# Performance work log

Hardware: AMD Instinct MI355X
Metric: run time of the kernel (lower is better)

Reference implementation:

```python
import jax, jax.numpy as jnp
import numpy as np

EPS = 1e-5
NUM_HEADS = 20


def ln(x, w, b=None):
    m = x.mean(-1, keepdims=True)
    v = x.var(-1, keepdims=True)
    y = (x - m) * jax.lax.rsqrt(v + EPS) * w
    return y + b if b is not None else y


def rotate_half(t):
    t1, t2 = jnp.split(t, 2, axis=-1)
    return jnp.concatenate([-t2, t1], axis=-1)


def setup_inputs() -> dict:
    key = jax.random.key(0)
    B, S, E = 8, 1024, 1280  # 8 packed sequences of length 1024, ESM-2 650M width
    T = B * S
    ks = jax.random.split(key, 6)
    scale = (1.0 / E) ** 0.5  # ~xavier scale
    w = lambda k: jax.random.normal(k, (E, E), jnp.float32) * scale
    return {
        "x": jax.random.normal(ks[0], (T, E), jnp.float32),
        "cu_lens": jnp.arange(B + 1, dtype=jnp.int32) * S,
        "max_len": S,
        "norm_w": jnp.ones((E,), jnp.float32),
        "norm_b": jnp.zeros((E,), jnp.float32),
        "Wq": w(ks[1]),
        "Wk": w(ks[2]),
        "Wv": w(ks[3]),
        "Wout": w(ks[4]),
        "lnq_w": jnp.ones((E,), jnp.float32),
        "lnk_w": jnp.ones((E,), jnp.float32),
    }


def reference(x, cu_lens, max_len, norm_w, norm_b, Wq, Wk, Wv, Wout, lnq_w, lnk_w):
    T, E = x.shape
    H = NUM_HEADS
    D = E // H

    # pre-norm + separate Q/K/V projections (bias=False)
    h = ln(x, norm_w, norm_b)
    q = ln(h @ Wq.T, lnq_w)   # per-head-stack LayerNorm on q (no bias)
    k = ln(h @ Wk.T, lnk_w)
    v = h @ Wv.T

    q = q.reshape(T, H, D)
    k = k.reshape(T, H, D)
    v = v.reshape(T, H, D)

    # rotary embedding: positions restart at each sequence boundary (cu_lens)
    tok = jnp.arange(T)
    seg = jnp.searchsorted(cu_lens, tok, side="right") - 1
    pos = (tok - cu_lens[seg]).astype(jnp.float32)
    inv_freq = 1.0 / (10000.0 ** (jnp.arange(0, D, 2, dtype=jnp.float32) / D))
    f = pos[:, None] * inv_freq[None, :]                      # [T, D/2]
    cos = jnp.concatenate([jnp.cos(f), jnp.cos(f)], -1)[:, None, :]  # [T,1,D]
    sin = jnp.concatenate([jnp.sin(f), jnp.sin(f)], -1)[:, None, :]
    q = q * cos + rotate_half(q) * sin
    k = k * cos + rotate_half(k) * sin

    # varlen flash attention; sequences are equal-length here so reshape to
    # [B,S,...] which exactly honors the block-diagonal (no cross-sequence) mask
    B = cu_lens.shape[0] - 1
    S = T // B
    qb = q.reshape(B, S, H, D)
    kb = k.reshape(B, S, H, D)
    vb = v.reshape(B, S, H, D)

    scores = jnp.einsum("bqhd,bkhd->bhqk", qb, kb) * (D ** -0.5)
    attn = jax.nn.softmax(scores, axis=-1)
    o = jnp.einsum("bhqk,bkhd->bqhd", attn, vb).reshape(T, E)
    return o @ Wout.T
```

## Files before the change

kernel.cpp:

```cpp
#include <hip/hip_runtime.h>
#include <hip/hip_bf16.h>
#include <math.h>

#define NH 20
#define HD 64
#define E_DIM 1280
#define T_TOK 8192
#define NSEQ 8
#define N4 (E_DIM * E_DIM / 4)

#define SCALE_LOG2 0.1803368801111204f
#define THR_RAW 44.3614f

typedef unsigned short u16;
typedef unsigned int u32;
typedef __attribute__((ext_vector_type(8))) short bf16x8;
typedef __attribute__((ext_vector_type(4))) float f32x4;
typedef __attribute__((ext_vector_type(16))) float f32x16;

__device__ __forceinline__ float bf2f(u16 h) {
  union { float f; unsigned u; } c; c.u = ((unsigned)h) << 16; return c.f;
}
__device__ __forceinline__ u16 f2bf(float f) {
  union { float f; unsigned u; } c; c.f = f;
  unsigned u = c.u;
  return (u16)((u + 0x7fffu + ((u >> 16) & 1u)) >> 16);
}
__device__ __forceinline__ u32 cvtpk(float lo, float hi) {
  u32 r;
  asm("v_cvt_pk_bf16_f32 %0, %1, %2" : "=v"(r) : "v"(lo), "v"(hi));
  return r;
}

__device__ __forceinline__ void gld_lds16(const void* g, void* l) {
  __builtin_amdgcn_global_load_lds((const __attribute__((address_space(1))) void*)g,
                                   (__attribute__((address_space(3))) void*)l,
                                   16, 0, 0);
}

__global__ __launch_bounds__(256) void cvt_all(const float* __restrict__ Wq,
                                               const float* __restrict__ Wk,
                                               const float* __restrict__ Wv,
                                               const float* __restrict__ Wo,
                                               u16* __restrict__ wqkv,
                                               u16* __restrict__ wo) {
  int i = blockIdx.x * 256 + threadIdx.x;
  if (i >= 4 * N4) return;
  int r = i / N4;
  int l = i - r * N4;
  const float* src = (r == 0) ? Wq : (r == 1) ? Wk : (r == 2) ? Wv : Wo;
  float4 v = ((const float4*)src)[l];
  ushort4 ov;
  ov.x = f2bf(v.x); ov.y = f2bf(v.y); ov.z = f2bf(v.z); ov.w = f2bf(v.w);
  if (r < 3) ((ushort4*)wqkv)[(size_t)r * N4 + l] = ov;
  else       ((ushort4*)wo)[l] = ov;
}

__global__ __launch_bounds__(256) void rope_tab_kernel(float2* __restrict__ tab) {
  int i = blockIdx.x * 256 + threadIdx.x;
  if (i >= 1024 * 32) return;
  int pos = i >> 5, dm = i & 31;
  float freq = exp2f(-(float)dm * (13.287712379549449f / 32.0f));
  float f = (float)pos * freq;
  tab[i] = make_float2(cosf(f), sinf(f));
}

__global__ __launch_bounds__(320) void ln_x_kernel(const float* __restrict__ x,
                                                   const float* __restrict__ w,
                                                   const float* __restrict__ b,
                                                   u16* __restrict__ h) {
  const int row = blockIdx.x;
  const int tid = threadIdx.x;
  const float4 xv = ((const float4*)(x + (size_t)row * E_DIM))[tid];
  float s  = xv.x + xv.y + xv.z + xv.w;
  float s2 = xv.x*xv.x + xv.y*xv.y + xv.z*xv.z + xv.w*xv.w;
#pragma unroll
  for (int m = 1; m < 64; m <<= 1) { s += __shfl_xor(s, m); s2 += __shfl_xor(s2, m); }
  __shared__ float ss[5], ss2[5];
  if ((tid & 63) == 0) { ss[tid >> 6] = s; ss2[tid >> 6] = s2; }
  __syncthreads();
  s  = ss[0] + ss[1] + ss[2] + ss[3] + ss[4];
  s2 = ss2[0] + ss2[1] + ss2[2] + ss2[3] + ss2[4];
  const float mean = s * (1.0f / E_DIM);
  const float var  = s2 * (1.0f / E_DIM) - mean * mean;
  const float rstd = rsqrtf(var + 1e-5f);
  const float4 wv = ((const float4*)w)[tid];
  const float4 bv = ((const float4*)b)[tid];
  ushort4 o;
  o.x = f2bf((xv.x - mean) * rstd * wv.x + bv.x);
  o.y = f2bf((xv.y - mean) * rstd * wv.y + bv.y);
  o.z = f2bf((xv.z - mean) * rstd * wv.z + bv.z);
  o.w = f2bf((xv.w - mean) * rstd * wv.w + bv.w);
  ((ushort4*)(h + (size_t)row * E_DIM))[tid] = o;
}

__global__ __launch_bounds__(320) void ln_rope_kernel(const u16* __restrict__ pre,
                                                      const float* __restrict__ w,
                                                      const int* __restrict__ cu,
                                                      const float2* __restrict__ tab,
                                                      u16* __restrict__ outq) {
  const int row = blockIdx.x;
  const int tid = threadIdx.x;
  __shared__ float y[E_DIM];
  const ushort4 qv = ((const ushort4*)(pre + (size_t)row * E_DIM))[tid];
  float v0 = bf2f(qv.x), v1 = bf2f(qv.y), v2 = bf2f(qv.z), v3 = bf2f(qv.w);
  float s  = v0 + v1 + v2 + v3;
  float s2 = v0*v0 + v1*v1 + v2*v2 + v3*v3;
#pragma unroll
  for (int m = 1; m < 64; m <<= 1) { s += __shfl_xor(s, m); s2 += __shfl_xor(s2, m); }
  __shared__ float ss[5], ss2[5];
  if ((tid & 63) == 0) { ss[tid >> 6] = s; ss2[tid >> 6] = s2; }
  __syncthreads();
  s  = ss[0] + ss[1] + ss[2] + ss[3] + ss[4];
  s2 = ss2[0] + ss2[1] + ss2[2] + ss2[3] + ss2[4];
  const float mean = s * (1.0f / E_DIM);
  const float var  = s2 * (1.0f / E_DIM) - mean * mean;
  const float rstd = rsqrtf(var + 1e-5f);
  const int e0 = tid * 4;
  const float4 wv = ((const float4*)w)[tid];
  y[e0 + 0] = (v0 - mean) * rstd * wv.x;
  y[e0 + 1] = (v1 - mean) * rstd * wv.y;
  y[e0 + 2] = (v2 - mean) * rstd * wv.z;
  y[e0 + 3] = (v3 - mean) * rstd * wv.w;
  __syncthreads();
  int seg = 0;
#pragma unroll
  for (int bb = 1; bb < NSEQ + 1; bb++) if (cu[bb] <= row) seg = bb;
  const int pos = row - cu[seg];
  const int d0 = e0 & 63;
  const int hbase = e0 - d0;
  const float4* tp = (const float4*)(tab + pos * 32 + (d0 & 31));
  const float4 t0 = tp[0], t1 = tp[1];
  const float cs_[4] = {t0.x, t0.z, t1.x, t1.z};
  const float sn_[4] = {t0.y, t0.w, t1.y, t1.w};
  const bool lo = (d0 < 32);
  ushort4 o;
#pragma unroll
  for (int i = 0; i < 4; i++) {
    const int d = d0 + i;
    float r;
    if (lo) r = y[hbase + d] * cs_[i] - y[hbase + d + 32] * sn_[i];
    else    r = y[hbase + d] * cs_[i] + y[hbase + d - 32] * sn_[i];
    ((u16*)&o)[i] = f2bf(r);
  }
  ((ushort4*)(outq + (size_t)row * E_DIM))[tid] = o;
}

__global__ __launch_bounds__(256) void gemm_qkv(const u16* __restrict__ A,
                                                const u16* __restrict__ B,
                                                u16* __restrict__ preq,
                                                u16* __restrict__ prek,
                                                u16* __restrict__ vT) {
  __shared__ u16 As[128 * 64];
  __shared__ u16 Bs[128 * 64];
  const int K = E_DIM;
  const int tid = threadIdx.x;
  const int wid = tid >> 6;
  const int lane = tid & 63;
  const int l16 = lane & 15, lq = lane >> 4;
  const int bm = blockIdx.x & 63;
  const int bn = blockIdx.x >> 6;
  const int m0 = bm << 7, n0 = bn << 7;
  const int wr = (wid >> 1) << 6;
  const int wc = (wid & 1) << 6;

  f32x4 acc[4][4] = {};
  const int rbase = tid >> 3;
  const int csw = (((tid & 7) ^ ((tid >> 3) & 7)) << 3);
  const int sw = l16 & 7;
  const int ldst = (wid << 6) * 8;

  for (int k0 = 0; k0 < K; k0 += 64) {
#pragma unroll
    for (int j = 0; j < 4; j++) {
      const int row = j * 32 + rbase;
      gld_lds16(A + (size_t)(m0 + row) * K + k0 + csw, &As[(size_t)(j * 2048) + ldst]);
      gld_lds16(B + (size_t)(n0 + row) * K + k0 + csw, &Bs[(size_t)(j * 2048) + ldst]);
    }
    __syncthreads();
#pragma unroll
    for (int kk = 0; kk < 2; kk++) {
      bf16x8 af[4], bfr[4];
#pragma unroll
      for (int mi = 0; mi < 4; mi++)
        af[mi] = *(const bf16x8*)(&As[(wr + mi * 16 + l16) * 64 + ((((kk << 2) | lq) ^ sw) << 3)]);
#pragma unroll
      for (int ni = 0; ni < 4; ni++)
        bfr[ni] = *(const bf16x8*)(&Bs[(wc + ni * 16 + l16) * 64 + ((((kk << 2) | lq) ^ sw) << 3)]);
#pragma unroll
      for (int mi = 0; mi < 4; mi++)
#pragma unroll
        for (int ni = 0; ni < 4; ni++)
          acc[mi][ni] = __builtin_amdgcn_mfma_f32_16x16x32_bf16(af[mi], bfr[ni], acc[mi][ni], 0, 0, 0);
    }
    __syncthreads();
  }

  if (n0 < 2560) {
    u16* dst; int c0;
    if (n0 < 1280) { dst = preq; c0 = n0; }
    else           { dst = prek; c0 = n0 - 1280; }
#pragma unroll
    for (int mi = 0; mi < 4; mi++)
#pragma unroll
      for (int j = 0; j < 4; j++) {
        const size_t rowo = (size_t)(m0 + wr + mi * 16 + lq * 4 + j) * E_DIM;
#pragma unroll
        for (int ni = 0; ni < 4; ni++)
          dst[rowo + c0 + wc + ni * 16 + l16] = f2bf(acc[mi][ni][j]);
      }
  } else {
    const int c0 = n0 - 2560;
#pragma unroll
    for (int mi = 0; mi < 4; mi++)
#pragma unroll
      for (int ni = 0; ni < 4; ni++) {
        ushort4 pkt;
        pkt.x = f2bf(acc[mi][ni][0]); pkt.y = f2bf(acc[mi][ni][1]);
        pkt.z = f2bf(acc[mi][ni][2]); pkt.w = f2bf(acc[mi][ni][3]);
        const size_t off = (size_t)(c0 + wc + ni * 16 + l16) * T_TOK + (m0 + wr + mi * 16 + lq * 4);
        *(ushort4*)(vT + off) = pkt;
      }
  }
}

__global__ __launch_bounds__(256) void gemm_out(const u16* __restrict__ A,
                                                const u16* __restrict__ B,
                                                float* __restrict__ C) {
  __shared__ u16 As[128 * 64];
  __shared__ u16 Bs[128 * 64];
  const int K = E_DIM, N = E_DIM;
  const int tid = threadIdx.x;
  const int wid = tid >> 6;
  const int lane = tid & 63;
  const int l16 = lane & 15, lq = lane >> 4;
  const int bm = blockIdx.x & 63;
  const int bn = blockIdx.x >> 6;
  const int m0 = bm << 7, n0 = bn << 7;
  const int wr = (wid >> 1) << 6;
  const int wc = (wid & 1) << 6;

  f32x4 acc[4][4] = {};
  const int rbase = tid >> 3;
  const int csw = (((tid & 7) ^ ((tid >> 3) & 7)) << 3);
  const int sw = l16 & 7;
  const int ldst = (wid << 6) * 8;

  for (int k0 = 0; k0 < K; k0 += 64) {
#pragma unroll
    for (int j = 0; j < 4; j++) {
      const int row = j * 32 + rbase;
      gld_lds16(A + (size_t)(m0 + row) * K + k0 + csw, &As[(size_t)(j * 2048) + ldst]);
      gld_lds16(B + (size_t)(n0 + row) * K + k0 + csw, &Bs[(size_t)(j * 2048) + ldst]);
    }
    __syncthreads();
#pragma unroll
    for (int kk = 0; kk < 2; kk++) {
      bf16x8 af[4], bfr[4];
#pragma unroll
      for (int mi = 0; mi < 4; mi++)
        af[mi] = *(const bf16x8*)(&As[(wr + mi * 16 + l16) * 64 + ((((kk << 2) | lq) ^ sw) << 3)]);
#pragma unroll
      for (int ni = 0; ni < 4; ni++)
        bfr[ni] = *(const bf16x8*)(&Bs[(wc + ni * 16 + l16) * 64 + ((((kk << 2) | lq) ^ sw) << 3)]);
#pragma unroll
      for (int mi = 0; mi < 4; mi++)
#pragma unroll
        for (int ni = 0; ni < 4; ni++)
          acc[mi][ni] = __builtin_amdgcn_mfma_f32_16x16x32_bf16(af[mi], bfr[ni], acc[mi][ni], 0, 0, 0);
    }
    __syncthreads();
  }

#pragma unroll
  for (int mi = 0; mi < 4; mi++)
#pragma unroll
    for (int j = 0; j < 4; j++) {
      const size_t rowo = (size_t)(m0 + wr + mi * 16 + lq * 4 + j) * N;
#pragma unroll
      for (int ni = 0; ni < 4; ni++)
        C[rowo + n0 + wc + ni * 16 + l16] = acc[mi][ni][j];
    }
}

__global__ __launch_bounds__(256) void attn_kernel(const u16* __restrict__ q,
                                                   const u16* __restrict__ k,
                                                   const u16* __restrict__ vT,
                                                   const int* __restrict__ cu,
                                                   u16* __restrict__ o) {
  const int bx = blockIdx.x;
  const int qt = bx & 7;
  const int hh = (bx >> 3) % NH;
  const int b  = bx / (8 * NH);
  const int base = cu[b];
  const int nkt  = (cu[b + 1] - base) >> 6;
  const int tid  = threadIdx.x;
  const int wid  = tid >> 6, lane = tid & 63;
  const int l31  = lane & 31, hi = lane >> 5;

  __shared__ u16 Ks[2][64 * 64];
  __shared__ u16 Vs[2][64 * 64];

  const int qrow = base + qt * 128 + wid * 32 + l31;
  bf16x8 qf[4];
#pragma unroll
  for (int kk = 0; kk < 4; kk++)
    qf[kk] = *(const bf16x8*)(q + (size_t)qrow * E_DIM + hh * 64 + kk * 16 + hi * 8);

  f32x16 acc0 = {}, acc1 = {};
  float mrow = -1e30f, lrow = 0.f;

  const int r0 = tid >> 3;
  const int chs = tid & 7;
  const int cs0 = (chs ^ (r0 & 7)) << 3;
  const int r1 = r0 + 32;
  const int cs1 = (chs ^ (r1 & 7)) << 3;
  const u16* kg0 = k  + (size_t)(base + r0) * E_DIM + hh * 64 + cs0;
  const u16* kg1 = k  + (size_t)(base + r1) * E_DIM + hh * 64 + cs1;
  const u16* vg0 = vT + (size_t)(hh * 64 + r0) * T_TOK + base + cs0;
  const u16* vg1 = vT + (size_t)(hh * 64 + r1) * T_TOK + base + cs1;
  const int ldsoff = wid * 512;

  gld_lds16(kg0, &Ks[0][ldsoff]);
  gld_lds16(kg1, &Ks[0][2048 + ldsoff]);
  gld_lds16(vg0, &Vs[0][ldsoff]);
  gld_lds16(vg1, &Vs[0][2048 + ldsoff]);
  __syncthreads();

  int cur = 0;
  for (int kt = 0; kt < nkt; kt++) {
    if (kt + 1 < nkt) {
      const size_t ko = (size_t)(kt + 1) * 64 * E_DIM;
      const int vo = (kt + 1) * 64;
      u16* kd = Ks[cur ^ 1];
      u16* vd = Vs[cur ^ 1];
      gld_lds16(kg0 + ko, kd + ldsoff);
      gld_lds16(kg1 + ko, kd + 2048 + ldsoff);
      gld_lds16(vg0 + vo, vd + ldsoff);
      gld_lds16(vg1 + vo, vd + 2048 + ldsoff);
    }
    const u16* Kc = Ks[cur];
    const u16* Vc = Vs[cur];

    f32x16 S0 = {}, S1 = {};
#pragma unroll
    for (int kk = 0; kk < 4; kk++) {
      const int c0 = (((kk << 1) | hi) ^ (l31 & 7)) << 3;
      const bf16x8 kf0 = *(const bf16x8*)(Kc + l31 * 64 + c0);
      const bf16x8 kf1 = *(const bf16x8*)(Kc + (32 + l31) * 64 + c0);
      S0 = __builtin_amdgcn_mfma_f32_32x32x16_bf16(kf0, qf[kk], S0, 0, 0, 0);
      S1 = __builtin_amdgcn_mfma_f32_32x32x16_bf16(kf1, qf[kk], S1, 0, 0, 0);
    }

    float tm = S0[0];
#pragma unroll
    for (int r = 1; r < 16; r++) tm = fmaxf(tm, S0[r]);
#pragma unroll
    for (int r = 0; r < 16; r++) tm = fmaxf(tm, S1[r]);
    tm = fmaxf(tm, __shfl_xor(tm, 32));

    if (__any(tm > mrow + THR_RAW)) {
      const float nm = fmaxf(mrow, tm);
      const float al = exp2f((mrow - nm) * SCALE_LOG2);
      mrow = nm;
      lrow *= al;
#pragma unroll
      for (int r = 0; r < 16; r++) {
        const float as = __shfl(al, (r & 3) + 8 * (r >> 2) + 4 * hi);
        acc0[r] *= as;
        acc1[r] *= as;
      }
    }
    const float ms = mrow * SCALE_LOG2;
    float rs = 0.f;
#pragma unroll
    for (int r = 0; r < 16; r++) {
      S0[r] = exp2f(fmaf(S0[r], SCALE_LOG2, -ms));
      rs += S0[r];
    }
#pragma unroll
    for (int r = 0; r < 16; r++) {
      S1[r] = exp2f(fmaf(S1[r], SCALE_LOG2, -ms));
      rs += S1[r];
    }
    rs += __shfl_xor(rs, 32);
    lrow += rs;

    u32 pw[4][4];
#pragma unroll
    for (int ks = 0; ks < 4; ks++) {
      const int g = (ks & 1) << 3;
      u32 A0, A1, B0, B1;
      if (ks < 2) {
        A0 = cvtpk(S0[g + 0], S0[g + 1]); A1 = cvtpk(S0[g + 2], S0[g + 3]);
        B0 = cvtpk(S0[g + 4], S0[g + 5]); B1 = cvtpk(S0[g + 6], S0[g + 7]);
      } else {
        A0 = cvtpk(S1[g + 0], S1[g + 1]); A1 = cvtpk(S1[g + 2], S1[g + 3]);
        B0 = cvtpk(S1[g + 4], S1[g + 5]); B1 = cvtpk(S1[g + 6], S1[g + 7]);
      }
      asm("v_permlane32_swap_b32 %0, %1" : "+v"(A0), "+v"(B0));
      asm("v_permlane32_swap_b32 %0, %1" : "+v"(A1), "+v"(B1));
      pw[ks][0] = A0; pw[ks][1] = A1; pw[ks][2] = B0; pw[ks][3] = B1;
    }

#pragma unroll
    for (int ks = 0; ks < 4; ks++) {
      const bf16x8 pa = *(const bf16x8*)&pw[ks][0];
      const int c0 = (((ks << 1) | hi) ^ (l31 & 7)) << 3;
      const bf16x8 vf0 = *(const bf16x8*)(Vc + l31 * 64 + c0);
      const bf16x8 vf1 = *(const bf16x8*)(Vc + (32 + l31) * 64 + c0);
      acc0 = __builtin_amdgcn_mfma_f32_32x32x16_bf16(pa, vf0, acc0, 0, 0, 0);
      acc1 = __builtin_amdgcn_mfma_f32_32x32x16_bf16(pa, vf1, acc1, 0, 0, 0);
    }
    __syncthreads();
    cur ^= 1;
  }

  const float linv = 1.0f / lrow;
  const int tok0 = base + qt * 128 + wid * 32;
#pragma unroll
  for (int r = 0; r < 16; r++) {
    const int qr = (r & 3) + 8 * (r >> 2) + 4 * hi;
    const float ls = __shfl(linv, qr);
    const size_t ro = (size_t)(tok0 + qr) * E_DIM + hh * 64 + l31;
    o[ro]      = f2bf(acc0[r] * ls);
    o[ro + 32] = f2bf(acc1[r] * ls);
  }
}

extern "C" void kernel_launch(void* const* d_in, const int* in_sizes, int n_in,
                              void* d_out, int out_size, void* d_ws, size_t ws_size,
                              hipStream_t stream) {
  const float* x      = (const float*)d_in[0];
  const int*   cu     = (const int*)d_in[1];
  const float* norm_w = (const float*)d_in[3];
  const float* norm_b = (const float*)d_in[4];
  const float* Wq     = (const float*)d_in[5];
  const float* Wk     = (const float*)d_in[6];
  const float* Wv     = (const float*)d_in[7];
  const float* Wo     = (const float*)d_in[8];
  const float* lnq    = (const float*)d_in[9];
  const float* lnk    = (const float*)d_in[10];
  float* out = (float*)d_out;

  const size_t EE2 = (size_t)E_DIM * E_DIM * 2;
  const size_t TE2 = (size_t)T_TOK * E_DIM * 2;
  char* p = (char*)d_ws;
  u16* wqkv = (u16*)p; p += 3 * EE2;
  u16* wo_b = (u16*)p; p += EE2;
  u16* h_b  = (u16*)p; p += TE2;
  u16* preq = (u16*)p; p += TE2;
  u16* prek = (u16*)p; p += TE2;
  u16* vT_b = (u16*)p; p += TE2;
  float2* tab = (float2*)p; p += 1024 * 32 * sizeof(float2);

  cvt_all<<<(4 * N4 + 255) / 256, 256, 0, stream>>>(Wq, Wk, Wv, Wo, wqkv, wo_b);
  rope_tab_kernel<<<128, 256, 0, stream>>>(tab);
  ln_x_kernel<<<T_TOK, 320, 0, stream>>>(x, norm_w, norm_b, h_b);

  gemm_qkv<<<64 * 30, 256, 0, stream>>>(h_b, wqkv, preq, prek, vT_b);

  ln_rope_kernel<<<T_TOK, 320, 0, stream>>>(preq, lnq, cu, tab, preq);
  ln_rope_kernel<<<T_TOK, 320, 0, stream>>>(prek, lnk, cu, tab, prek);

  attn_kernel<<<8 * NH * NSEQ, 256, 0, stream>>>(preq, prek, vT_b, cu, h_b);

  gemm_out<<<64 * 10, 256, 0, stream>>>(h_b, wo_b, out);
}
```

Baseline: 297.2 us.

## Replace both GEMMs with 256x256 double-buffered 8-wave pipelined template

Merges the QKV and output projection GEMMs into one templated kernel with 256x256 tiles, 512 threads and double-buffered LDS. Global-to-LDS loads are interleaved with MFMA quarter-blocks under explicit vmcnt/lgkmcnt waits, barriers and setprio. The goal is to hide load latency and raise data reuse per block. In exchange it uses 128KB of LDS per block with fewer blocks, and the out GEMM launches only 160 blocks on a chip with 256 CUs, which leaves many CUs idle.

```diff
diff --git a/kernel.cpp b/kernel.cpp
--- a/kernel.cpp
+++ b/kernel.cpp
@@ -37,6 +37,12 @@
                                    (__attribute__((address_space(3))) void*)l,
                                    16, 0, 0);
 }
+
+#define BARR() __builtin_amdgcn_s_barrier()
+#define LGKM0() do { asm volatile("s_waitcnt lgkmcnt(0)" ::: "memory"); \
+                     __builtin_amdgcn_sched_barrier(0); } while (0)
+#define VMC4() asm volatile("s_waitcnt vmcnt(4)" ::: "memory")
+#define VMC0() asm volatile("s_waitcnt vmcnt(0)" ::: "memory")
 
 __global__ __launch_bounds__(256) void cvt_all(const float* __restrict__ Wq,
                                                const float* __restrict__ Wk,
@@ -146,141 +152,150 @@
   ((ushort4*)(outq + (size_t)row * E_DIM))[tid] = o;
 }
 
-__global__ __launch_bounds__(256) void gemm_qkv(const u16* __restrict__ A,
-                                                const u16* __restrict__ B,
-                                                u16* __restrict__ preq,
-                                                u16* __restrict__ prek,
-                                                u16* __restrict__ vT) {
-  __shared__ u16 As[128 * 64];
-  __shared__ u16 Bs[128 * 64];
-  const int K = E_DIM;
+template <int MODE, int K>
+__global__ __launch_bounds__(512) void gemm256(const u16* __restrict__ A,
+                                               const u16* __restrict__ B,
+                                               u16* __restrict__ preq,
+                                               u16* __restrict__ prek,
+                                               u16* __restrict__ vT,
+                                               float* __restrict__ Cf) {
+  __shared__ u16 As[2][16384];
+  __shared__ u16 Bs[2][16384];
   const int tid = threadIdx.x;
-  const int wid = tid >> 6;
-  const int lane = tid & 63;
+  const int wid = tid >> 6, lane = tid & 63;
   const int l16 = lane & 15, lq = lane >> 4;
-  const int bm = blockIdx.x & 63;
-  const int bn = blockIdx.x >> 6;
-  const int m0 = bm << 7, n0 = bn << 7;
-  const int wr = (wid >> 1) << 6;
-  const int wc = (wid & 1) << 6;
-
-  f32x4 acc[4][4] = {};
-  const int rbase = tid >> 3;
-  const int csw = (((tid & 7) ^ ((tid >> 3) & 7)) << 3);
+  const int wm = wid >> 2, wn = wid & 3;
+  const int bm = blockIdx.x & 31;
+  const int bn = blockIdx.x >> 5;
+  const int m0 = bm << 8, n0 = bn << 8;
   const int sw = l16 & 7;
-  const int ldst = (wid << 6) * 8;
-
-  for (int k0 = 0; k0 < K; k0 += 64) {
-#pragma unroll
-    for (int j = 0; j < 4; j++) {
-      const int row = j * 32 + rbase;
-      gld_lds16(A + (size_t)(m0 + row) * K + k0 + csw, &As[(size_t)(j * 2048) + ldst]);
-      gld_lds16(B + (size_t)(n0 + row) * K + k0 + csw, &Bs[(size_t)(j * 2048) + ldst]);
-    }
-    __syncthreads();
-#pragma unroll
-    for (int kk = 0; kk < 2; kk++) {
-      bf16x8 af[4], bfr[4];
-#pragma unroll
-      for (int mi = 0; mi < 4; mi++)
-        af[mi] = *(const bf16x8*)(&As[(wr + mi * 16 + l16) * 64 + ((((kk << 2) | lq) ^ sw) << 3)]);
-#pragma unroll
-      for (int ni = 0; ni < 4; ni++)
-        bfr[ni] = *(const bf16x8*)(&Bs[(wc + ni * 16 + l16) * 64 + ((((kk << 2) | lq) ^ sw) << 3)]);
-#pragma unroll
-      for (int mi = 0; mi < 4; mi++)
+
+  const int row0 = tid >> 3;
+  const int ch0 = ((tid & 7) ^ (row0 & 7)) << 3;
+  const u16* Abase = A + (size_t)(m0 + row0) * K + ch0;
+  const u16* Bbase = B + (size_t)(n0 + row0) * K + ch0;
+  const int dst0 = tid * 8;
+
+  const int CA = (wm * 128 + l16) * 64;
+  const int CB = (wn * 64 + l16) * 64;
+  const int ch_0 = ((0 | lq) ^ sw) << 3;
+  const int ch_1 = ((4 | lq) ^ sw) << 3;
+
+  f32x4 acc[8][4] = {};
+  bf16x8 aF[4][2], bF[2][2][2];
+
+#define STG(Larr, bufp, hh, gbase, kt) do {                                     \
+    const u16* g_ = (gbase) + (size_t)(hh) * 128 * K + (size_t)(kt) * 64;       \
+    gld_lds16(g_, &Larr[bufp][(hh) * 8192 + dst0]);                             \
+    gld_lds16(g_ + (size_t)64 * K, &Larr[bufp][(hh) * 8192 + dst0 + 4096]);     \
+  } while (0)
+
+#define RDA(bufp, a) do {                                                       \
+    _Pragma("unroll") for (int mb = 0; mb < 4; mb++) {                          \
+      aF[mb][0] = *(const bf16x8*)(&As[bufp][CA + (a) * 4096 + mb * 1024 + ch_0]); \
+      aF[mb][1] = *(const bf16x8*)(&As[bufp][CA + (a) * 4096 + mb * 1024 + ch_1]); \
+    } } while (0)
+
+#define RDB(bufp, b) do {                                                       \
+    _Pragma("unroll") for (int nb = 0; nb < 2; nb++) {                          \
+      bF[b][nb][0] = *(const bf16x8*)(&Bs[bufp][CB + (b) * 2048 + nb * 1024 + ch_0]); \
+      bF[b][nb][1] = *(const bf16x8*)(&Bs[bufp][CB + (b) * 2048 + nb * 1024 + ch_1]); \
+    } } while (0)
+
+#define MFQ(a, b) do {                                                          \
+    __builtin_amdgcn_s_setprio(1);                                              \
+    _Pragma("unroll") for (int mb = 0; mb < 4; mb++)                            \
+    _Pragma("unroll") for (int nb = 0; nb < 2; nb++)                            \
+    _Pragma("unroll") for (int kk = 0; kk < 2; kk++)                            \
+      acc[(a) * 4 + mb][(b) * 2 + nb] = __builtin_amdgcn_mfma_f32_16x16x32_bf16( \
+          aF[mb][kk], bF[b][nb][kk], acc[(a) * 4 + mb][(b) * 2 + nb], 0, 0, 0); \
+    __builtin_amdgcn_s_setprio(0); } while (0)
+
+  STG(Bs, 0, 0, Bbase, 0);
+  STG(As, 0, 0, Abase, 0);
+  STG(Bs, 0, 1, Bbase, 0);
+  STG(As, 0, 1, Abase, 0);
+  STG(Bs, 1, 0, Bbase, 1);
+  STG(As, 1, 0, Abase, 1);
+  VMC4();
+  BARR();
+
+  const int NIT = K / 128;
+  for (int i = 0; i < NIT; i++) {
+    const bool lastI = (i == NIT - 1);
+    const int k1 = 2 * i + 1, k2 = 2 * i + 2, k3 = 2 * i + 3;
+    RDA(0, 0); RDB(0, 0);
+    STG(Bs, 1, 1, Bbase, k1);
+    BARR(); LGKM0(); MFQ(0, 0); BARR();
+    RDB(0, 1);
+    STG(As, 1, 1, Abase, k1);
+    BARR(); LGKM0(); MFQ(0, 1); BARR();
+    RDA(0, 1);
+    if (!lastI) STG(Bs, 0, 0, Bbase, k2);
+    BARR(); LGKM0(); MFQ(1, 0); BARR();
+    if (!lastI) { STG(As, 0, 0, Abase, k2); VMC4(); } else { VMC0(); }
+    BARR(); LGKM0(); MFQ(1, 1); BARR();
+    RDA(1, 0); RDB(1, 0);
+    if (!lastI) STG(Bs, 0, 1, Bbase, k2);
+    BARR(); LGKM0(); MFQ(0, 0); BARR();
+    RDB(1, 1);
+    if (!lastI) STG(As, 0, 1, Abase, k2);
+    BARR(); LGKM0(); MFQ(0, 1); BARR();
+    RDA(1, 1);
+    if (!lastI) STG(Bs, 1, 0, Bbase, k3);
+    BARR(); LGKM0(); MFQ(1, 0); BARR();
+    if (!lastI) {
+      STG(As, 1, 0, Abase, k3);
+      VMC4();
+      BARR(); LGKM0(); MFQ(1, 1); BARR();
+    } else {
+      LGKM0(); MFQ(1, 1);
+    }
+  }
+#undef STG
+#undef RDA
+#undef RDB
+#undef MFQ
+
+  if (MODE == 0) {
+    if (n0 < 2560) {
+      u16* dst; int c0;
+      if (n0 < 1280) { dst = preq; c0 = n0; }
+      else           { dst = prek; c0 = n0 - 1280; }
+#pragma unroll
+      for (int mi = 0; mi < 8; mi++)
+#pragma unroll
+        for (int j = 0; j < 4; j++) {
+          const size_t rowo = (size_t)(m0 + wm * 128 + mi * 16 + lq * 4 + j) * E_DIM;
+#pragma unroll
+          for (int ni = 0; ni < 4; ni++)
+            dst[rowo + c0 + wn * 64 + ni * 16 + l16] = f2bf(acc[mi][ni][j]);
+        }
+    } else {
+      const int c0 = n0 - 2560;
+#pragma unroll
+      for (int mi = 0; mi < 8; mi++)
+#pragma unroll
+        for (int ni = 0; ni < 4; ni++) {
+          ushort4 pkt;
+          pkt.x = f2bf(acc[mi][ni][0]); pkt.y = f2bf(acc[mi][ni][1]);
+          pkt.z = f2bf(acc[mi][ni][2]); pkt.w = f2bf(acc[mi][ni][3]);
+          const size_t off = (size_t)(c0 + wn * 64 + ni * 16 + l16) * T_TOK +
+                             (m0 + wm * 128 + mi * 16 + lq * 4);
+          *(ushort4*)(vT + off) = pkt;
+        }
+    }
+  } else {
+#pragma unroll
+    for (int mi = 0; mi < 8; mi++)
+#pragma unroll
+      for (int j = 0; j < 4; j++) {
+        const size_t rowo = (size_t)(m0 + wm * 128 + mi * 16 + lq * 4 + j) * E_DIM;
 #pragma unroll
         for (int ni = 0; ni < 4; ni++)
-          acc[mi][ni] = __builtin_amdgcn_mfma_f32_16x16x32_bf16(af[mi], bfr[ni], acc[mi][ni], 0, 0, 0);
-    }
-    __syncthreads();
-  }
-
-  if (n0 < 2560) {
-    u16* dst; int c0;
-    if (n0 < 1280) { dst = preq; c0 = n0; }
-    else           { dst = prek; c0 = n0 - 1280; }
-#pragma unroll
-    for (int mi = 0; mi < 4; mi++)
-#pragma unroll
-      for (int j = 0; j < 4; j++) {
-        const size_t rowo = (size_t)(m0 + wr + mi * 16 + lq * 4 + j) * E_DIM;
-#pragma unroll
-        for (int ni = 0; ni < 4; ni++)
-          dst[rowo + c0 + wc + ni * 16 + l16] = f2bf(acc[mi][ni][j]);
-      }
-  } else {
-    const int c0 = n0 - 2560;
-#pragma unroll
-    for (int mi = 0; mi < 4; mi++)
-#pragma unroll
-      for (int ni = 0; ni < 4; ni++) {
-        ushort4 pkt;
-        pkt.x = f2bf(acc[mi][ni][0]); pkt.y = f2bf(acc[mi][ni][1]);
-        pkt.z = f2bf(acc[mi][ni][2]); pkt.w = f2bf(acc[mi][ni][3]);
-        const size_t off = (size_t)(c0 + wc + ni * 16 + l16) * T_TOK + (m0 + wr + mi * 16 + lq * 4);
-        *(ushort4*)(vT + off) = pkt;
+          Cf[rowo + n0 + wn * 64 + ni * 16 + l16] = acc[mi][ni][j];
       }
   }
-}
-
-__global__ __launch_bounds__(256) void gemm_out(const u16* __restrict__ A,
-                                                const u16* __restrict__ B,
-                                                float* __restrict__ C) {
-  __shared__ u16 As[128 * 64];
-  __shared__ u16 Bs[128 * 64];
-  const int K = E_DIM, N = E_DIM;
-  const int tid = threadIdx.x;
-  const int wid = tid >> 6;
-  const int lane = tid & 63;
-  const int l16 = lane & 15, lq = lane >> 4;
-  const int bm = blockIdx.x & 63;
-  const int bn = blockIdx.x >> 6;
-  const int m0 = bm << 7, n0 = bn << 7;
-  const int wr = (wid >> 1) << 6;
-  const int wc = (wid & 1) << 6;
-
-  f32x4 acc[4][4] = {};
-  const int rbase = tid >> 3;
-  const int csw = (((tid & 7) ^ ((tid >> 3) & 7)) << 3);
-  const int sw = l16 & 7;
-  const int ldst = (wid << 6) * 8;
-
-  for (int k0 = 0; k0 < K; k0 += 64) {
-#pragma unroll
-    for (int j = 0; j < 4; j++) {
-      const int row = j * 32 + rbase;
-      gld_lds16(A + (size_t)(m0 + row) * K + k0 + csw, &As[(size_t)(j * 2048) + ldst]);
-      gld_lds16(B + (size_t)(n0 + row) * K + k0 + csw, &Bs[(size_t)(j * 2048) + ldst]);
-    }
-    __syncthreads();
-#pragma unroll
-    for (int kk = 0; kk < 2; kk++) {
-      bf16x8 af[4], bfr[4];
-#pragma unroll
-      for (int mi = 0; mi < 4; mi++)
-        af[mi] = *(const bf16x8*)(&As[(wr + mi * 16 + l16) * 64 + ((((kk << 2) | lq) ^ sw) << 3)]);
-#pragma unroll
-      for (int ni = 0; ni < 4; ni++)
-        bfr[ni] = *(const bf16x8*)(&Bs[(wc + ni * 16 + l16) * 64 + ((((kk << 2) | lq) ^ sw) << 3)]);
-#pragma unroll
-      for (int mi = 0; mi < 4; mi++)
-#pragma unroll
-        for (int ni = 0; ni < 4; ni++)
-          acc[mi][ni] = __builtin_amdgcn_mfma_f32_16x16x32_bf16(af[mi], bfr[ni], acc[mi][ni], 0, 0, 0);
-    }
-    __syncthreads();
-  }
-
-#pragma unroll
-  for (int mi = 0; mi < 4; mi++)
-#pragma unroll
-    for (int j = 0; j < 4; j++) {
-      const size_t rowo = (size_t)(m0 + wr + mi * 16 + lq * 4 + j) * N;
-#pragma unroll
-      for (int ni = 0; ni < 4; ni++)
-        C[rowo + n0 + wc + ni * 16 + l16] = acc[mi][ni][j];
-    }
 }
 
 __global__ __launch_bounds__(256) void attn_kernel(const u16* __restrict__ q,
@@ -458,12 +473,12 @@
   rope_tab_kernel<<<128, 256, 0, stream>>>(tab);
   ln_x_kernel<<<T_TOK, 320, 0, stream>>>(x, norm_w, norm_b, h_b);
 
-  gemm_qkv<<<64 * 30, 256, 0, stream>>>(h_b, wqkv, preq, prek, vT_b);
+  gemm256<0, E_DIM><<<480, 512, 0, stream>>>(h_b, wqkv, preq, prek, vT_b, nullptr);
 
   ln_rope_kernel<<<T_TOK, 320, 0, stream>>>(preq, lnq, cu, tab, preq);
   ln_rope_kernel<<<T_TOK, 320, 0, stream>>>(prek, lnk, cu, tab, prek);
 
   attn_kernel<<<8 * NH * NSEQ, 256, 0, stream>>>(preq, prek, vT_b, cu, h_b);
 
-  gemm_out<<<64 * 10, 256, 0, stream>>>(h_b, wo_b, out);
-}
+  gemm256<1, E_DIM><<<160, 512, 0, stream>>>(h_b, wo_b, nullptr, nullptr, nullptr, out);
+}
```

Result: faster. 282.4 us (-5.0%).
